# Performance work log

Measured on AMD Instinct MI355X. Metric: run time of the kernel, lower is better.

The kernel has to match this reference:

```python
import jax, jax.numpy as jnp
import numpy as np

B, N, H, C = 8, 128, 768, 5


def setup_inputs() -> dict:
    key = jax.random.key(0)
    k0, k1, k2, k3 = jax.random.split(key, 4)
    h = jax.random.normal(k0, (B, N, H), dtype=jnp.float32)
    # torch nn.Linear(4H, H): out = x @ W.T + b; we store Wcat = W.T with shape [4H, H]
    Wcat = jax.random.normal(k1, (4 * H, H), dtype=jnp.float32) * 0.02
    bW = jnp.zeros((H,), dtype=jnp.float32)
    h_hat = jax.random.normal(k2, (H,), dtype=jnp.float32)
    Wout = jax.random.normal(k3, (H, C), dtype=jnp.float32) * 0.02
    bout = jnp.zeros((C,), dtype=jnp.float32)
    return {"h": h, "Wcat": Wcat, "bW": bW, "h_hat": h_hat, "Wout": Wout, "bout": bout}


def reference(h, Wcat, bW, h_hat, Wout, bout):
    n = h.shape[1]
    W1, W2, W3, W4 = jnp.split(Wcat, 4, axis=0)  # each [H, H]
    # span order matches the torch double loop: i in range(N), j in range(i, N)
    ii, jj = jnp.triu_indices(n)  # P = n(n+1)/2
    # cat([hi,hj,hi-hj,hi*hj]) @ Wcat == hi@(W1+W3) + hj@(W2-W3) + (hi*hj)@W4
    A = jnp.einsum('bnh,hk->bnk', h, W1 + W3)   # [B, N, H]
    Bm = jnp.einsum('bnh,hk->bnk', h, W2 - W3)  # [B, N, H]
    prod = h[:, ii, :] * h[:, jj, :]            # [B, P, H]
    spans = jnp.tanh(A[:, ii, :] + Bm[:, jj, :]
                     + jnp.einsum('bph,hk->bpk', prod, W4) + bW)  # [B, P, H]
    # InterpretationLayer: attention pooling over spans
    alpha = jax.nn.softmax(jnp.einsum('bph,h->bp', spans, h_hat), axis=1)
    h_tilde = jnp.einsum('bp,bph->bh', alpha, spans)  # [B, H]
    logits = h_tilde @ Wout + bout                    # [B, C]
    return jax.nn.log_softmax(logits, axis=1)
```

## Files before the change

kernel.cpp:

```cpp
#include <hip/hip_runtime.h>
#include <hip/hip_bf16.h>


#define B_ 8
#define N_ 128
#define H_ 768
#define C_ 5
#define P_ 8256
#define TP 64
#define NBLK 129

typedef short bf16x8 __attribute__((ext_vector_type(8)));
typedef float f32x4 __attribute__((ext_vector_type(4)));

__device__ __forceinline__ float bf2f(unsigned short u){
  union { unsigned u; float f; } v; v.u = ((unsigned)u) << 16; return v.f;
}
__device__ __forceinline__ unsigned short f2bf(float f){
  union { float f; unsigned u; } v; v.f = f;
  unsigned r = v.u + 0x7FFFu + ((v.u >> 16) & 1u);
  return (unsigned short)(r >> 16);
}
__device__ __forceinline__ float tanh_fast(float x){
  float e = __expf(2.f * x);
  return 1.f - 2.f / (e + 1.f);
}
__device__ __forceinline__ int lds_off(int row, int k){
  return row * (H_ * 2) + ((k * 2) ^ ((row & 7) << 4));
}


#define PH_BLKS 3072
#define PW_BLKS 288
#define PR_BLKS 33

__global__ void prep(const float* __restrict__ h, const float* __restrict__ Wcat,
                     unsigned short* __restrict__ hb,
                     unsigned short* __restrict__ Wsum,
                     unsigned short* __restrict__ Wdif,
                     unsigned short* __restrict__ W4s,
                     int* __restrict__ ii, int* __restrict__ jj){
  const int bid = blockIdx.x;
  if (bid < PH_BLKS){
    int idx = bid * 256 + threadIdx.x;
    hb[idx] = f2bf(h[idx]);
  } else if (bid < PH_BLKS + PW_BLKS){
    int idx = (bid - PH_BLKS) * 256 + threadIdx.x;
    int o = idx / H_, col = idx % H_;
    bf16x8 vs, vd, v4;
    #pragma unroll
    for (int e = 0; e < 8; e++){
      int hrow = o * 8 + e;
      float w1 = Wcat[hrow * H_ + col];
      float w2 = Wcat[(H_ + hrow) * H_ + col];
      float w3 = Wcat[(2 * H_ + hrow) * H_ + col];
      float w4 = Wcat[(3 * H_ + hrow) * H_ + col];
      vs[e] = (short)f2bf(w1 + w3);
      vd[e] = (short)f2bf(w2 - w3);
      v4[e] = (short)f2bf(w4);
    }
    int pbase = (o * H_ + col) * 8;
    *(bf16x8*)(Wsum + pbase) = vs;
    *(bf16x8*)(Wdif + pbase) = vd;
    *(bf16x8*)(W4s + pbase)  = v4;
  } else {
    int p = (bid - PH_BLKS - PW_BLKS) * 256 + threadIdx.x;
    if (p < P_){
      int i = 0, off = 0;
      while (off + (N_ - i) <= p){ off += (N_ - i); i++; }
      ii[p] = i; jj[p] = i + (p - off);
    }
  }
}


__global__ __launch_bounds__(512, 4) void coef_gemm(
    const unsigned short* __restrict__ hb,
    const unsigned short* __restrict__ Wsum,
    const unsigned short* __restrict__ Wdif,
    const float* __restrict__ bW,
    float* __restrict__ Acoef, float* __restrict__ Bcoef){
  const int sel = blockIdx.y;
  const unsigned short* Wp = sel ? Wdif : Wsum;
  float* out = sel ? Bcoef : Acoef;
  const int growb = blockIdx.x * 16;

  __shared__ char As[16 * H_ * 2];

  const int tid = threadIdx.x;
  {
    int r = tid >> 5;
    int c = tid & 31;
    const unsigned short* src = hb + (growb + r) * H_;
    #pragma unroll
    for (int kk = 0; kk < 3; kk++){
      int k = kk * 256 + c * 8;
      bf16x8 v = *(const bf16x8*)(src + k);
      *(bf16x8*)(As + lds_off(r, k)) = v;
    }
  }
  __syncthreads();

  const int lane = tid & 63;
  const int wn = tid >> 6;
  const int hi = lane >> 4;
  const int l15 = lane & 15;
  const int colbase = wn * 96 + l15;

  f32x4 acc[6] = {};

  const bf16x8* wp = (const bf16x8*)Wp + hi * H_ + colbase;
  bf16x8 bc0 = wp[0], bc1 = wp[16], bc2 = wp[32], bc3 = wp[48], bc4 = wp[64], bc5 = wp[80];
  wp += 4 * H_;
  for (int step = 0; step < 24; ++step){
    bf16x8 bn0 = wp[0], bn1 = wp[16], bn2 = wp[32], bn3 = wp[48], bn4 = wp[64], bn5 = wp[80];
    wp += 4 * H_;
    bf16x8 a = *(const bf16x8*)(As + lds_off(l15, step * 32 + hi * 8));
    acc[0] = __builtin_amdgcn_mfma_f32_16x16x32_bf16(a, bc0, acc[0], 0, 0, 0);
    acc[1] = __builtin_amdgcn_mfma_f32_16x16x32_bf16(a, bc1, acc[1], 0, 0, 0);
    acc[2] = __builtin_amdgcn_mfma_f32_16x16x32_bf16(a, bc2, acc[2], 0, 0, 0);
    acc[3] = __builtin_amdgcn_mfma_f32_16x16x32_bf16(a, bc3, acc[3], 0, 0, 0);
    acc[4] = __builtin_amdgcn_mfma_f32_16x16x32_bf16(a, bc4, acc[4], 0, 0, 0);
    acc[5] = __builtin_amdgcn_mfma_f32_16x16x32_bf16(a, bc5, acc[5], 0, 0, 0);
    bc0 = bn0; bc1 = bn1; bc2 = bn2; bc3 = bn3; bc4 = bn4; bc5 = bn5;
  }

  #pragma unroll
  for (int ni = 0; ni < 6; ni++){
    int col = colbase + ni * 16;
    float bw = (sel == 0) ? bW[col] : 0.f;
    #pragma unroll
    for (int r = 0; r < 4; r++){
      int grow = growb + hi * 4 + r;
      out[grow * H_ + col] = acc[ni][r] + bw;
    }
  }
}


__global__ __launch_bounds__(1024)
__attribute__((amdgpu_waves_per_eu(4, 4)))
void spans_fused(
    const unsigned short* __restrict__ hb,
    const float* __restrict__ Acoef,
    const float* __restrict__ Bcoef,
    const unsigned short* __restrict__ W4s,
    const float* __restrict__ hhat,
    const int* __restrict__ ii,
    const int* __restrict__ jj,
    float* __restrict__ pm, float* __restrict__ pl, float* __restrict__ pacc){
  __shared__ char As[TP * H_ * 2];
  __shared__ int iis[TP], jjs[TP];
  __shared__ float sbuf[16][TP];
  __shared__ float wbuf[TP];

  const int bid = blockIdx.x;
  const int b = bid / NBLK;
  const int p0 = (bid % NBLK) * TP;
  const int tid = threadIdx.x;

  if (tid < TP){ iis[tid] = ii[p0 + tid]; jjs[tid] = jj[p0 + tid]; }
  __syncthreads();

  {
    int r = tid >> 4;
    int c = tid & 15;
    const unsigned short* hp = hb + (b * N_ + iis[r]) * H_;
    const unsigned short* hq = hb + (b * N_ + jjs[r]) * H_;
    #pragma unroll
    for (int kk = 0; kk < 6; kk++){
      int k = kk * 128 + c * 8;
      bf16x8 va = *(const bf16x8*)(hp + k);
      bf16x8 vb = *(const bf16x8*)(hq + k);
      bf16x8 vp;
      #pragma unroll
      for (int e = 0; e < 8; e++)
        vp[e] = (short)f2bf(bf2f((unsigned short)va[e]) * bf2f((unsigned short)vb[e]));
      *(bf16x8*)(As + lds_off(r, k)) = vp;
    }
  }

  const int lane = tid & 63;
  const int wave = tid >> 6;
  const int hi = lane >> 4;
  const int l15 = lane & 15;
  const int colbase = wave * 48 + l15;

  f32x4 acc[4][3];
  #pragma unroll
  for (int mi = 0; mi < 4; mi++){
    #pragma unroll
    for (int r = 0; r < 4; r++){
      int rowl = mi * 16 + hi * 4 + r;
      const float* ap = Acoef + (b * N_ + iis[rowl]) * H_ + colbase;
      const float* bp = Bcoef + (b * N_ + jjs[rowl]) * H_ + colbase;
      #pragma unroll
      for (int ni = 0; ni < 3; ni++)
        acc[mi][ni][r] = ap[ni * 16] + bp[ni * 16];
    }
  }
  __syncthreads();

  const bf16x8* wp = (const bf16x8*)W4s + hi * H_ + colbase;
  bf16x8 bc0 = wp[0], bc1 = wp[16], bc2 = wp[32];
  wp += 4 * H_;
  for (int step = 0; step < 24; ++step){
    bf16x8 bn0 = wp[0], bn1 = wp[16], bn2 = wp[32];
    wp += 4 * H_;
    const int kb = step * 32 + hi * 8;
    bf16x8 a0 = *(const bf16x8*)(As + lds_off(     l15, kb));
    bf16x8 a1 = *(const bf16x8*)(As + lds_off(16 + l15, kb));
    bf16x8 a2 = *(const bf16x8*)(As + lds_off(32 + l15, kb));
    bf16x8 a3 = *(const bf16x8*)(As + lds_off(48 + l15, kb));
    acc[0][0] = __builtin_amdgcn_mfma_f32_16x16x32_bf16(a0, bc0, acc[0][0], 0, 0, 0);
    acc[1][0] = __builtin_amdgcn_mfma_f32_16x16x32_bf16(a1, bc0, acc[1][0], 0, 0, 0);
    acc[2][0] = __builtin_amdgcn_mfma_f32_16x16x32_bf16(a2, bc0, acc[2][0], 0, 0, 0);
    acc[3][0] = __builtin_amdgcn_mfma_f32_16x16x32_bf16(a3, bc0, acc[3][0], 0, 0, 0);
    acc[0][1] = __builtin_amdgcn_mfma_f32_16x16x32_bf16(a0, bc1, acc[0][1], 0, 0, 0);
    acc[1][1] = __builtin_amdgcn_mfma_f32_16x16x32_bf16(a1, bc1, acc[1][1], 0, 0, 0);
    acc[2][1] = __builtin_amdgcn_mfma_f32_16x16x32_bf16(a2, bc1, acc[2][1], 0, 0, 0);
    acc[3][1] = __builtin_amdgcn_mfma_f32_16x16x32_bf16(a3, bc1, acc[3][1], 0, 0, 0);
    acc[0][2] = __builtin_amdgcn_mfma_f32_16x16x32_bf16(a0, bc2, acc[0][2], 0, 0, 0);
    acc[1][2] = __builtin_amdgcn_mfma_f32_16x16x32_bf16(a1, bc2, acc[1][2], 0, 0, 0);
    acc[2][2] = __builtin_amdgcn_mfma_f32_16x16x32_bf16(a2, bc2, acc[2][2], 0, 0, 0);
    acc[3][2] = __builtin_amdgcn_mfma_f32_16x16x32_bf16(a3, bc2, acc[3][2], 0, 0, 0);
    bc0 = bn0; bc1 = bn1; bc2 = bn2;
  }

  float sc[4][4];
  #pragma unroll
  for (int mi = 0; mi < 4; mi++)
    #pragma unroll
    for (int r = 0; r < 4; r++) sc[mi][r] = 0.f;

  #pragma unroll
  for (int ni = 0; ni < 3; ni++){
    float hh = hhat[colbase + ni * 16];
    #pragma unroll
    for (int mi = 0; mi < 4; mi++){
      #pragma unroll
      for (int r = 0; r < 4; r++){
        float s = tanh_fast(acc[mi][ni][r]);
        acc[mi][ni][r] = s;
        sc[mi][r] += s * hh;
      }
    }
  }
  #pragma unroll
  for (int mi = 0; mi < 4; mi++)
    #pragma unroll
    for (int r = 0; r < 4; r++){
      float v = sc[mi][r];
      v += __shfl_xor(v, 1); v += __shfl_xor(v, 2);
      v += __shfl_xor(v, 4); v += __shfl_xor(v, 8);
      sc[mi][r] = v;
    }
  if (l15 == 0){
    #pragma unroll
    for (int mi = 0; mi < 4; mi++)
      #pragma unroll
      for (int r = 0; r < 4; r++)
        sbuf[wave][mi * 16 + hi * 4 + r] = sc[mi][r];
  }
  __syncthreads();

  if (tid < TP){
    float s = 0.f;
    #pragma unroll
    for (int w = 0; w < 16; w++) s += sbuf[w][tid];
    float m = s;
    #pragma unroll
    for (int off = 1; off < 64; off <<= 1) m = fmaxf(m, __shfl_xor(m, off));
    float w = __expf(s - m);
    float l = w;
    #pragma unroll
    for (int off = 1; off < 64; off <<= 1) l += __shfl_xor(l, off);
    wbuf[tid] = w;
    if (tid == 0){ pm[bid] = m; pl[bid] = l; }
  }
  __syncthreads();

  #pragma unroll
  for (int ni = 0; ni < 3; ni++){
    float wa = 0.f;
    #pragma unroll
    for (int mi = 0; mi < 4; mi++)
      #pragma unroll
      for (int r = 0; r < 4; r++){
        int rowl = mi * 16 + hi * 4 + r;
        wa += wbuf[rowl] * acc[mi][ni][r];
      }
    wa += __shfl_xor(wa, 16);
    wa += __shfl_xor(wa, 32);
    if (lane < 16) pacc[bid * H_ + colbase + ni * 16] = wa;
  }
}


__global__ void merge1(
    const float* __restrict__ pm, const float* __restrict__ pl,
    const float* __restrict__ pacc, float* __restrict__ htg){
  __shared__ float ebuf[NBLK];
  __shared__ float Msh, invLsh;
  __shared__ float part[128];
  const int b = blockIdx.x;
  const int ch = blockIdx.y;
  const int tid = threadIdx.x;

  if (tid < 64){
    float m = -3.4e38f;
    for (int t = tid; t < NBLK; t += 64) m = fmaxf(m, pm[b * NBLK + t]);
    #pragma unroll
    for (int off = 1; off < 64; off <<= 1) m = fmaxf(m, __shfl_xor(m, off));
    float l = 0.f;
    for (int t = tid; t < NBLK; t += 64) l += pl[b * NBLK + t] * __expf(pm[b * NBLK + t] - m);
    #pragma unroll
    for (int off = 1; off < 64; off <<= 1) l += __shfl_xor(l, off);
    if (tid == 0){ Msh = m; invLsh = 1.f / l; }
  }
  __syncthreads();
  if (tid < NBLK) ebuf[tid] = __expf(pm[b * NBLK + tid] - Msh);
  __syncthreads();
  const int col = ch * 128 + (tid & 127);
  const int half = tid >> 7;
  float a = 0.f;
  for (int t = half; t < NBLK; t += 2) a += pacc[(b * NBLK + t) * H_ + col] * ebuf[t];
  if (half) part[tid & 127] = a;
  __syncthreads();
  if (!half) htg[b * H_ + col] = (a + part[tid]) * invLsh;
}


__global__ void merge2(
    const float* __restrict__ htg,
    const float* __restrict__ Wout, const float* __restrict__ bout,
    float* __restrict__ outp){
  const int b = blockIdx.x;
  const int lane = threadIdx.x;
  float a[C_] = {};
  for (int k = lane; k < H_; k += 64){
    float hv = htg[b * H_ + k];
    #pragma unroll
    for (int c = 0; c < C_; c++) a[c] += hv * Wout[k * C_ + c];
  }
  #pragma unroll
  for (int c = 0; c < C_; c++){
    #pragma unroll
    for (int off = 1; off < 64; off <<= 1) a[c] += __shfl_xor(a[c], off);
  }
  if (lane == 0){
    float lg[C_];
    #pragma unroll
    for (int c = 0; c < C_; c++) lg[c] = a[c] + bout[c];
    float mx = lg[0];
    #pragma unroll
    for (int c = 1; c < C_; c++) mx = fmaxf(mx, lg[c]);
    float s = 0.f;
    #pragma unroll
    for (int c = 0; c < C_; c++) s += __expf(lg[c] - mx);
    float ls = __logf(s) + mx;
    #pragma unroll
    for (int c = 0; c < C_; c++) outp[b * C_ + c] = lg[c] - ls;
  }
}


extern "C" void kernel_launch(void* const* d_in, const int* in_sizes, int n_in,
                              void* d_out, int out_size, void* d_ws, size_t ws_size,
                              hipStream_t stream){
  const float* h    = (const float*)d_in[0];
  const float* Wcat = (const float*)d_in[1];
  const float* bW   = (const float*)d_in[2];
  const float* hhat = (const float*)d_in[3];
  const float* Wout = (const float*)d_in[4];
  const float* bout = (const float*)d_in[5];
  float* outp = (float*)d_out;

  unsigned short* hb   = (unsigned short*)d_ws;
  unsigned short* Wsum = hb + 786432;
  unsigned short* Wdif = Wsum + 589824;
  unsigned short* W4s  = Wdif + 589824;
  float* Acoef = (float*)(W4s + 589824);
  float* Bcoef = Acoef + 786432;
  int* iiA = (int*)(Bcoef + 786432);
  int* jjA = iiA + P_;
  float* pm = (float*)(jjA + P_);
  float* pl = pm + (B_ * NBLK);
  float* pacc = pl + (B_ * NBLK);
  float* htg  = pacc + (B_ * NBLK * H_);

  prep<<<PH_BLKS + PW_BLKS + PR_BLKS, 256, 0, stream>>>(h, Wcat, hb, Wsum, Wdif, W4s, iiA, jjA);
  coef_gemm<<<dim3(64, 2), 512, 0, stream>>>(hb, Wsum, Wdif, bW, Acoef, Bcoef);
  spans_fused<<<B_ * NBLK, 1024, 0, stream>>>(hb, Acoef, Bcoef, W4s, hhat, iiA, jjA, pm, pl, pacc);
  merge1<<<dim3(B_, 6), 256, 0, stream>>>(pm, pl, pacc, htg);
  merge2<<<B_, 64, 0, stream>>>(htg, Wout, bout, outp);
}
```

Measured before the change: 183.6 us.

## Double-buffer span product slabs in LDS to overlap gather with MFMA

The kernel no longer builds the full 64x768 bf16 product tile in LDS before the matmul. It now splits K into three 256-wide slabs held in two LDS buffers, and loads the next slab's h rows from global memory while MFMAs run on the current one. This cuts LDS from 96KB to 64KB and hides the gather latency, at the cost of extra barriers per slab and more registers held live. The LDS swizzle also widens from 8 to 16 rows, and the launch bounds attribute is rewritten as launch_bounds(1024,4).

```diff
diff --git a/kernel.cpp b/kernel.cpp
--- a/kernel.cpp
+++ b/kernel.cpp
@@ -9,6 +9,8 @@
 #define P_ 8256
 #define TP 64
 #define NBLK 129
+#define KSLAB 256
+#define NSLAB 3
 
 typedef short bf16x8 __attribute__((ext_vector_type(8)));
 typedef float f32x4 __attribute__((ext_vector_type(4)));
@@ -26,7 +28,11 @@
   return 1.f - 2.f / (e + 1.f);
 }
 __device__ __forceinline__ int lds_off(int row, int k){
-  return row * (H_ * 2) + ((k * 2) ^ ((row & 7) << 4));
+  return row * (H_ * 2) + ((k * 2) ^ ((row & 15) << 4));
+}
+__device__ __forceinline__ int slab_off(int buf, int row, int klocal){
+  return buf * (TP * KSLAB * 2) + row * (KSLAB * 2)
+       + ((klocal * 2) ^ ((row & 15) << 4));
 }
 
 
@@ -138,8 +144,7 @@
 }
 
 
-__global__ __launch_bounds__(1024)
-__attribute__((amdgpu_waves_per_eu(4, 4)))
+__global__ __launch_bounds__(1024, 4)
 void spans_fused(
     const unsigned short* __restrict__ hb,
     const float* __restrict__ Acoef,
@@ -149,7 +154,7 @@
     const int* __restrict__ ii,
     const int* __restrict__ jj,
     float* __restrict__ pm, float* __restrict__ pl, float* __restrict__ pacc){
-  __shared__ char As[TP * H_ * 2];
+  __shared__ char As[2 * TP * KSLAB * 2];
   __shared__ int iis[TP], jjs[TP];
   __shared__ float sbuf[16][TP];
   __shared__ float wbuf[TP];
@@ -161,30 +166,22 @@
 
   if (tid < TP){ iis[tid] = ii[p0 + tid]; jjs[tid] = jj[p0 + tid]; }
   __syncthreads();
-
-  {
-    int r = tid >> 4;
-    int c = tid & 15;
-    const unsigned short* hp = hb + (b * N_ + iis[r]) * H_;
-    const unsigned short* hq = hb + (b * N_ + jjs[r]) * H_;
-    #pragma unroll
-    for (int kk = 0; kk < 6; kk++){
-      int k = kk * 128 + c * 8;
-      bf16x8 va = *(const bf16x8*)(hp + k);
-      bf16x8 vb = *(const bf16x8*)(hq + k);
-      bf16x8 vp;
-      #pragma unroll
-      for (int e = 0; e < 8; e++)
-        vp[e] = (short)f2bf(bf2f((unsigned short)va[e]) * bf2f((unsigned short)vb[e]));
-      *(bf16x8*)(As + lds_off(r, k)) = vp;
-    }
-  }
 
   const int lane = tid & 63;
   const int wave = tid >> 6;
   const int hi = lane >> 4;
   const int l15 = lane & 15;
   const int colbase = wave * 48 + l15;
+
+  const int r_st = tid >> 4;
+  const int c_st = tid & 15;
+  const unsigned short* hp = hb + (b * N_ + iis[r_st]) * H_;
+  const unsigned short* hq = hb + (b * N_ + jjs[r_st]) * H_;
+
+  bf16x8 va0 = *(const bf16x8*)(hp + c_st * 8);
+  bf16x8 va1 = *(const bf16x8*)(hp + 128 + c_st * 8);
+  bf16x8 vb0 = *(const bf16x8*)(hq + c_st * 8);
+  bf16x8 vb1 = *(const bf16x8*)(hq + 128 + c_st * 8);
 
   f32x4 acc[4][3];
   #pragma unroll
@@ -199,32 +196,68 @@
         acc[mi][ni][r] = ap[ni * 16] + bp[ni * 16];
     }
   }
+
+  {
+    bf16x8 vp0, vp1;
+    #pragma unroll
+    for (int e = 0; e < 8; e++){
+      vp0[e] = (short)f2bf(bf2f((unsigned short)va0[e]) * bf2f((unsigned short)vb0[e]));
+      vp1[e] = (short)f2bf(bf2f((unsigned short)va1[e]) * bf2f((unsigned short)vb1[e]));
+    }
+    *(bf16x8*)(As + slab_off(0, r_st, c_st * 8)) = vp0;
+    *(bf16x8*)(As + slab_off(0, r_st, 128 + c_st * 8)) = vp1;
+  }
   __syncthreads();
 
   const bf16x8* wp = (const bf16x8*)W4s + hi * H_ + colbase;
   bf16x8 bc0 = wp[0], bc1 = wp[16], bc2 = wp[32];
   wp += 4 * H_;
-  for (int step = 0; step < 24; ++step){
-    bf16x8 bn0 = wp[0], bn1 = wp[16], bn2 = wp[32];
-    wp += 4 * H_;
-    const int kb = step * 32 + hi * 8;
-    bf16x8 a0 = *(const bf16x8*)(As + lds_off(     l15, kb));
-    bf16x8 a1 = *(const bf16x8*)(As + lds_off(16 + l15, kb));
-    bf16x8 a2 = *(const bf16x8*)(As + lds_off(32 + l15, kb));
-    bf16x8 a3 = *(const bf16x8*)(As + lds_off(48 + l15, kb));
-    acc[0][0] = __builtin_amdgcn_mfma_f32_16x16x32_bf16(a0, bc0, acc[0][0], 0, 0, 0);
-    acc[1][0] = __builtin_amdgcn_mfma_f32_16x16x32_bf16(a1, bc0, acc[1][0], 0, 0, 0);
-    acc[2][0] = __builtin_amdgcn_mfma_f32_16x16x32_bf16(a2, bc0, acc[2][0], 0, 0, 0);
-    acc[3][0] = __builtin_amdgcn_mfma_f32_16x16x32_bf16(a3, bc0, acc[3][0], 0, 0, 0);
-    acc[0][1] = __builtin_amdgcn_mfma_f32_16x16x32_bf16(a0, bc1, acc[0][1], 0, 0, 0);
-    acc[1][1] = __builtin_amdgcn_mfma_f32_16x16x32_bf16(a1, bc1, acc[1][1], 0, 0, 0);
-    acc[2][1] = __builtin_amdgcn_mfma_f32_16x16x32_bf16(a2, bc1, acc[2][1], 0, 0, 0);
-    acc[3][1] = __builtin_amdgcn_mfma_f32_16x16x32_bf16(a3, bc1, acc[3][1], 0, 0, 0);
-    acc[0][2] = __builtin_amdgcn_mfma_f32_16x16x32_bf16(a0, bc2, acc[0][2], 0, 0, 0);
-    acc[1][2] = __builtin_amdgcn_mfma_f32_16x16x32_bf16(a1, bc2, acc[1][2], 0, 0, 0);
-    acc[2][2] = __builtin_amdgcn_mfma_f32_16x16x32_bf16(a2, bc2, acc[2][2], 0, 0, 0);
-    acc[3][2] = __builtin_amdgcn_mfma_f32_16x16x32_bf16(a3, bc2, acc[3][2], 0, 0, 0);
-    bc0 = bn0; bc1 = bn1; bc2 = bn2;
+
+  #pragma unroll
+  for (int slab = 0; slab < NSLAB; ++slab){
+    const int buf = slab & 1;
+    if (slab + 1 < NSLAB){
+      const int kg = (slab + 1) * KSLAB;
+      va0 = *(const bf16x8*)(hp + kg + c_st * 8);
+      va1 = *(const bf16x8*)(hp + kg + 128 + c_st * 8);
+      vb0 = *(const bf16x8*)(hq + kg + c_st * 8);
+      vb1 = *(const bf16x8*)(hq + kg + 128 + c_st * 8);
+    }
+    #pragma unroll
+    for (int st = 0; st < 8; ++st){
+      bf16x8 bn0{}, bn1{}, bn2{};
+      const bool haveNext = !(slab == NSLAB - 1 && st == 7);
+      if (haveNext){ bn0 = wp[0]; bn1 = wp[16]; bn2 = wp[32]; wp += 4 * H_; }
+      const int kl = st * 32 + hi * 8;
+      bf16x8 a0 = *(const bf16x8*)(As + slab_off(buf,      l15, kl));
+      bf16x8 a1 = *(const bf16x8*)(As + slab_off(buf, 16 + l15, kl));
+      bf16x8 a2 = *(const bf16x8*)(As + slab_off(buf, 32 + l15, kl));
+      bf16x8 a3 = *(const bf16x8*)(As + slab_off(buf, 48 + l15, kl));
+      acc[0][0] = __builtin_amdgcn_mfma_f32_16x16x32_bf16(a0, bc0, acc[0][0], 0, 0, 0);
+      acc[1][0] = __builtin_amdgcn_mfma_f32_16x16x32_bf16(a1, bc0, acc[1][0], 0, 0, 0);
+      acc[2][0] = __builtin_amdgcn_mfma_f32_16x16x32_bf16(a2, bc0, acc[2][0], 0, 0, 0);
+      acc[3][0] = __builtin_amdgcn_mfma_f32_16x16x32_bf16(a3, bc0, acc[3][0], 0, 0, 0);
+      acc[0][1] = __builtin_amdgcn_mfma_f32_16x16x32_bf16(a0, bc1, acc[0][1], 0, 0, 0);
+      acc[1][1] = __builtin_amdgcn_mfma_f32_16x16x32_bf16(a1, bc1, acc[1][1], 0, 0, 0);
+      acc[2][1] = __builtin_amdgcn_mfma_f32_16x16x32_bf16(a2, bc1, acc[2][1], 0, 0, 0);
+      acc[3][1] = __builtin_amdgcn_mfma_f32_16x16x32_bf16(a3, bc1, acc[3][1], 0, 0, 0);
+      acc[0][2] = __builtin_amdgcn_mfma_f32_16x16x32_bf16(a0, bc2, acc[0][2], 0, 0, 0);
+      acc[1][2] = __builtin_amdgcn_mfma_f32_16x16x32_bf16(a1, bc2, acc[1][2], 0, 0, 0);
+      acc[2][2] = __builtin_amdgcn_mfma_f32_16x16x32_bf16(a2, bc2, acc[2][2], 0, 0, 0);
+      acc[3][2] = __builtin_amdgcn_mfma_f32_16x16x32_bf16(a3, bc2, acc[3][2], 0, 0, 0);
+      bc0 = bn0; bc1 = bn1; bc2 = bn2;
+    }
+    if (slab + 1 < NSLAB){
+      bf16x8 vp0, vp1;
+      #pragma unroll
+      for (int e = 0; e < 8; e++){
+        vp0[e] = (short)f2bf(bf2f((unsigned short)va0[e]) * bf2f((unsigned short)vb0[e]));
+        vp1[e] = (short)f2bf(bf2f((unsigned short)va1[e]) * bf2f((unsigned short)vb1[e]));
+      }
+      *(bf16x8*)(As + slab_off(buf ^ 1, r_st, c_st * 8)) = vp0;
+      *(bf16x8*)(As + slab_off(buf ^ 1, r_st, 128 + c_st * 8)) = vp1;
+    }
+    __syncthreads();
   }
 
   float sc[4][4];
```

New measurement: 189.6 us. 1.03x slower.

## Stream W4 slabs into LDS via async global_load_lds with double-buffered product tiles

Applied to the files above, without the earlier changes.

Replaces the up-front construction of the full 64x768 product tile in LDS with a K-chunked, double-buffered pipeline. Each 32-wide K-slab of W4 is copied directly into LDS with global_load_lds while the current slab is consumed by MFMAs. The hi*hj products are now built per 128-wide chunk into a ping-pong LDS buffer, with the next chunk's loads issued ahead. The intent is to overlap weight and activation loads with matrix math, and to have each W4 slab fetched once per block into shared memory instead of per wave from global. In exchange there is a __syncthreads per step, and LDS use rises to roughly 96KB for the W4 slabs plus the product buffers. The swizzle also changes to use 16 rows, and the occupancy hint moves from waves_per_eu to launch_bounds.

```diff
diff --git a/kernel.cpp b/kernel.cpp
--- a/kernel.cpp
+++ b/kernel.cpp
@@ -9,6 +9,8 @@
 #define P_ 8256
 #define TP 64
 #define NBLK 129
+#define NSTEP 24
+#define BSLAB 49152
 
 typedef short bf16x8 __attribute__((ext_vector_type(8)));
 typedef float f32x4 __attribute__((ext_vector_type(4)));
@@ -25,8 +27,14 @@
   float e = __expf(2.f * x);
   return 1.f - 2.f / (e + 1.f);
 }
+__device__ __forceinline__ void gload_lds16(const char* g, char* l){
+  __builtin_amdgcn_global_load_lds(
+      (const __attribute__((address_space(1))) unsigned int*)g,
+      (__attribute__((address_space(3))) unsigned int*)l,
+      16, 0, 0);
+}
 __device__ __forceinline__ int lds_off(int row, int k){
-  return row * (H_ * 2) + ((k * 2) ^ ((row & 7) << 4));
+  return row * (H_ * 2) + ((k * 2) ^ ((row & 15) << 4));
 }
 
 
@@ -138,8 +146,7 @@
 }
 
 
-__global__ __launch_bounds__(1024)
-__attribute__((amdgpu_waves_per_eu(4, 4)))
+__global__ __launch_bounds__(1024, 4)
 void spans_fused(
     const unsigned short* __restrict__ hb,
     const float* __restrict__ Acoef,
@@ -149,7 +156,8 @@
     const int* __restrict__ ii,
     const int* __restrict__ jj,
     float* __restrict__ pm, float* __restrict__ pl, float* __restrict__ pacc){
-  __shared__ char As[TP * H_ * 2];
+  __shared__ char Pp[2][TP * 128 * 2];
+  __shared__ char Bsl[2][BSLAB];
   __shared__ int iis[TP], jjs[TP];
   __shared__ float sbuf[16][TP];
   __shared__ float wbuf[TP];
@@ -161,24 +169,6 @@
 
   if (tid < TP){ iis[tid] = ii[p0 + tid]; jjs[tid] = jj[p0 + tid]; }
   __syncthreads();
-
-  {
-    int r = tid >> 4;
-    int c = tid & 15;
-    const unsigned short* hp = hb + (b * N_ + iis[r]) * H_;
-    const unsigned short* hq = hb + (b * N_ + jjs[r]) * H_;
-    #pragma unroll
-    for (int kk = 0; kk < 6; kk++){
-      int k = kk * 128 + c * 8;
-      bf16x8 va = *(const bf16x8*)(hp + k);
-      bf16x8 vb = *(const bf16x8*)(hq + k);
-      bf16x8 vp;
-      #pragma unroll
-      for (int e = 0; e < 8; e++)
-        vp[e] = (short)f2bf(bf2f((unsigned short)va[e]) * bf2f((unsigned short)vb[e]));
-      *(bf16x8*)(As + lds_off(r, k)) = vp;
-    }
-  }
 
   const int lane = tid & 63;
   const int wave = tid >> 6;
@@ -186,6 +176,16 @@
   const int l15 = lane & 15;
   const int colbase = wave * 48 + l15;
 
+  const int r_st = tid >> 4;
+  const int c_st = tid & 15;
+  const unsigned short* hp = hb + (b * N_ + iis[r_st]) * H_;
+  const unsigned short* hq = hb + (b * N_ + jjs[r_st]) * H_;
+  const int pwoff = r_st * 256 + ((c_st * 16) ^ ((r_st & 15) << 4));
+  const char* wbase = (const char*)W4s;
+  const int bchunk = wave * 3072;
+
+  bf16x8 va = *(const bf16x8*)(hp + c_st * 8);
+  bf16x8 vb = *(const bf16x8*)(hq + c_st * 8);
   f32x4 acc[4][3];
   #pragma unroll
   for (int mi = 0; mi < 4; mi++){
@@ -199,32 +199,59 @@
         acc[mi][ni][r] = ap[ni * 16] + bp[ni * 16];
     }
   }
-  __syncthreads();
-
-  const bf16x8* wp = (const bf16x8*)W4s + hi * H_ + colbase;
-  bf16x8 bc0 = wp[0], bc1 = wp[16], bc2 = wp[32];
-  wp += 4 * H_;
-  for (int step = 0; step < 24; ++step){
-    bf16x8 bn0 = wp[0], bn1 = wp[16], bn2 = wp[32];
-    wp += 4 * H_;
-    const int kb = step * 32 + hi * 8;
-    bf16x8 a0 = *(const bf16x8*)(As + lds_off(     l15, kb));
-    bf16x8 a1 = *(const bf16x8*)(As + lds_off(16 + l15, kb));
-    bf16x8 a2 = *(const bf16x8*)(As + lds_off(32 + l15, kb));
-    bf16x8 a3 = *(const bf16x8*)(As + lds_off(48 + l15, kb));
-    acc[0][0] = __builtin_amdgcn_mfma_f32_16x16x32_bf16(a0, bc0, acc[0][0], 0, 0, 0);
-    acc[1][0] = __builtin_amdgcn_mfma_f32_16x16x32_bf16(a1, bc0, acc[1][0], 0, 0, 0);
-    acc[2][0] = __builtin_amdgcn_mfma_f32_16x16x32_bf16(a2, bc0, acc[2][0], 0, 0, 0);
-    acc[3][0] = __builtin_amdgcn_mfma_f32_16x16x32_bf16(a3, bc0, acc[3][0], 0, 0, 0);
-    acc[0][1] = __builtin_amdgcn_mfma_f32_16x16x32_bf16(a0, bc1, acc[0][1], 0, 0, 0);
-    acc[1][1] = __builtin_amdgcn_mfma_f32_16x16x32_bf16(a1, bc1, acc[1][1], 0, 0, 0);
-    acc[2][1] = __builtin_amdgcn_mfma_f32_16x16x32_bf16(a2, bc1, acc[2][1], 0, 0, 0);
-    acc[3][1] = __builtin_amdgcn_mfma_f32_16x16x32_bf16(a3, bc1, acc[3][1], 0, 0, 0);
-    acc[0][2] = __builtin_amdgcn_mfma_f32_16x16x32_bf16(a0, bc2, acc[0][2], 0, 0, 0);
-    acc[1][2] = __builtin_amdgcn_mfma_f32_16x16x32_bf16(a1, bc2, acc[1][2], 0, 0, 0);
-    acc[2][2] = __builtin_amdgcn_mfma_f32_16x16x32_bf16(a2, bc2, acc[2][2], 0, 0, 0);
-    acc[3][2] = __builtin_amdgcn_mfma_f32_16x16x32_bf16(a3, bc2, acc[3][2], 0, 0, 0);
-    bc0 = bn0; bc1 = bn1; bc2 = bn2;
+  {
+    bf16x8 vp;
+    #pragma unroll
+    for (int e = 0; e < 8; e++)
+      vp[e] = (short)f2bf(bf2f((unsigned short)va[e]) * bf2f((unsigned short)vb[e]));
+    *(bf16x8*)(Pp[0] + pwoff) = vp;
+  }
+  #pragma unroll
+  for (int t = 0; t < 3; t++)
+    gload_lds16(wbase + bchunk + t * 1024 + lane * 16,
+                Bsl[0] + bchunk + t * 1024);
+
+  for (int s = 0; s < NSTEP; ++s){
+    const int buf = s & 1;
+    const int pbuf = (s >> 2) & 1;
+    __syncthreads();
+
+    if (s < NSTEP - 1){
+      const char* src = wbase + (s + 1) * BSLAB + bchunk;
+      #pragma unroll
+      for (int t = 0; t < 3; t++)
+        gload_lds16(src + t * 1024 + lane * 16,
+                    Bsl[buf ^ 1] + bchunk + t * 1024);
+    }
+    if ((s & 3) == 0 && s + 4 < NSTEP){
+      const int kg = ((s >> 2) + 1) * 128;
+      va = *(const bf16x8*)(hp + kg + c_st * 8);
+      vb = *(const bf16x8*)(hq + kg + c_st * 8);
+    }
+
+    const int klb = (s & 3) * 64 + hi * 16;
+    const char* pp = Pp[pbuf];
+    bf16x8 a0 = *(const bf16x8*)(pp + (     l15) * 256 + (klb ^ (l15 << 4)));
+    bf16x8 a1 = *(const bf16x8*)(pp + (16 + l15) * 256 + (klb ^ (l15 << 4)));
+    bf16x8 a2 = *(const bf16x8*)(pp + (32 + l15) * 256 + (klb ^ (l15 << 4)));
+    bf16x8 a3 = *(const bf16x8*)(pp + (48 + l15) * 256 + (klb ^ (l15 << 4)));
+    const char* bb = Bsl[buf] + (hi * H_ + colbase) * 16;
+    #pragma unroll
+    for (int ni = 0; ni < 3; ni++){
+      bf16x8 bf = *(const bf16x8*)(bb + ni * 256);
+      acc[0][ni] = __builtin_amdgcn_mfma_f32_16x16x32_bf16(a0, bf, acc[0][ni], 0, 0, 0);
+      acc[1][ni] = __builtin_amdgcn_mfma_f32_16x16x32_bf16(a1, bf, acc[1][ni], 0, 0, 0);
+      acc[2][ni] = __builtin_amdgcn_mfma_f32_16x16x32_bf16(a2, bf, acc[2][ni], 0, 0, 0);
+      acc[3][ni] = __builtin_amdgcn_mfma_f32_16x16x32_bf16(a3, bf, acc[3][ni], 0, 0, 0);
+    }
+
+    if ((s & 3) == 3 && s < NSTEP - 1){
+      bf16x8 vp;
+      #pragma unroll
+      for (int e = 0; e < 8; e++)
+        vp[e] = (short)f2bf(bf2f((unsigned short)va[e]) * bf2f((unsigned short)vb[e]));
+      *(bf16x8*)(Pp[pbuf ^ 1] + pwoff) = vp;
+    }
   }
 
   float sc[4][4];
```

Result: slower. 199.9 us (+8.9%).

## Retile span kernel to 96-row tiles with double-buffered K-slab product staging

Applied to the files above, without the earlier changes.

The span GEMM kernel now processes 96 spans per block with 512 threads. Each wave computes a 96x96 output tile using a 6x6 accumulator grid, so W4 fragments are reused across more rows. The hi*hj product is no longer staged fully up front: it goes into LDS in 128-wide K slabs with double buffering, so the next slab is loaded and converted while the MFMAs run on the current one. A packed bf16 convert instruction, MFMA priority hints and a two-pass softmax over 96 rows are also added. The change trades higher register pressure (144 accumulator floats per lane) and fewer blocks (688 instead of 1032) for fewer W4 reloads per span.

```diff
diff --git a/kernel.cpp b/kernel.cpp
--- a/kernel.cpp
+++ b/kernel.cpp
@@ -7,8 +7,11 @@
 #define H_ 768
 #define C_ 5
 #define P_ 8256
-#define TP 64
-#define NBLK 129
+#define TP 96
+#define NBLK 86
+#define NSTEP 24
+#define SLABK 128
+#define NSLAB 6
 
 typedef short bf16x8 __attribute__((ext_vector_type(8)));
 typedef float f32x4 __attribute__((ext_vector_type(4)));
@@ -25,8 +28,20 @@
   float e = __expf(2.f * x);
   return 1.f - 2.f / (e + 1.f);
 }
+__device__ __forceinline__ bf16x8 prodpack(bf16x8 x, bf16x8 y){
+  union { bf16x8 v; unsigned u[4]; } o;
+  #pragma unroll
+  for (int e2 = 0; e2 < 4; e2++){
+    float p0 = bf2f((unsigned short)x[e2*2])   * bf2f((unsigned short)y[e2*2]);
+    float p1 = bf2f((unsigned short)x[e2*2+1]) * bf2f((unsigned short)y[e2*2+1]);
+    unsigned pk;
+    asm volatile("v_cvt_pk_bf16_f32 %0, %1, %2" : "=v"(pk) : "v"(p0), "v"(p1));
+    o.u[e2] = pk;
+  }
+  return o.v;
+}
 __device__ __forceinline__ int lds_off(int row, int k){
-  return row * (H_ * 2) + ((k * 2) ^ ((row & 7) << 4));
+  return row * (H_ * 2) + ((k * 2) ^ ((row & 15) << 4));
 }
 
 
@@ -138,8 +153,29 @@
 }
 
 
-__global__ __launch_bounds__(1024)
-__attribute__((amdgpu_waves_per_eu(4, 4)))
+#define STEP_BODY(T, BCUR, BNXT)                                             \
+  {                                                                          \
+    if ((T) + 1 < NSTEP){                                                    \
+      _Pragma("unroll")                                                      \
+      for (int ni = 0; ni < 6; ni++)                                         \
+        BNXT[ni] = wp[(((T) + 1) * 4 + hi) * H_ + colbase + ni * 16];        \
+    }                                                                        \
+    const int klb = ((T) & 3) * 64 + hi * 16;                                \
+    bf16x8 a[6];                                                             \
+    _Pragma("unroll")                                                        \
+    for (int mg = 0; mg < 6; mg++)                                           \
+      a[mg] = *(const bf16x8*)(pcur + (mg * 16 + l15) * 256 + (klb ^ (l15 << 4))); \
+    __builtin_amdgcn_s_setprio(1);                                           \
+    _Pragma("unroll")                                                        \
+    for (int ni = 0; ni < 6; ni++){                                          \
+      _Pragma("unroll")                                                      \
+      for (int mg = 0; mg < 6; mg++)                                         \
+        acc[mg][ni] = __builtin_amdgcn_mfma_f32_16x16x32_bf16(a[mg], BCUR[ni], acc[mg][ni], 0, 0, 0); \
+    }                                                                        \
+    __builtin_amdgcn_s_setprio(0);                                           \
+  }
+
+__global__ __launch_bounds__(512, 2)
 void spans_fused(
     const unsigned short* __restrict__ hb,
     const float* __restrict__ Acoef,
@@ -149,10 +185,11 @@
     const int* __restrict__ ii,
     const int* __restrict__ jj,
     float* __restrict__ pm, float* __restrict__ pl, float* __restrict__ pacc){
-  __shared__ char As[TP * H_ * 2];
+  __shared__ char Pp[2][TP * 256];
   __shared__ int iis[TP], jjs[TP];
-  __shared__ float sbuf[16][TP];
+  __shared__ float sbuf[8][TP];
   __shared__ float wbuf[TP];
+  __shared__ float Msh;
 
   const int bid = blockIdx.x;
   const int b = bid / NBLK;
@@ -162,134 +199,147 @@
   if (tid < TP){ iis[tid] = ii[p0 + tid]; jjs[tid] = jj[p0 + tid]; }
   __syncthreads();
 
-  {
-    int r = tid >> 4;
-    int c = tid & 15;
-    const unsigned short* hp = hb + (b * N_ + iis[r]) * H_;
-    const unsigned short* hq = hb + (b * N_ + jjs[r]) * H_;
-    #pragma unroll
-    for (int kk = 0; kk < 6; kk++){
-      int k = kk * 128 + c * 8;
-      bf16x8 va = *(const bf16x8*)(hp + k);
-      bf16x8 vb = *(const bf16x8*)(hq + k);
-      bf16x8 vp;
-      #pragma unroll
-      for (int e = 0; e < 8; e++)
-        vp[e] = (short)f2bf(bf2f((unsigned short)va[e]) * bf2f((unsigned short)vb[e]));
-      *(bf16x8*)(As + lds_off(r, k)) = vp;
-    }
-  }
-
   const int lane = tid & 63;
   const int wave = tid >> 6;
   const int hi = lane >> 4;
   const int l15 = lane & 15;
-  const int colbase = wave * 48 + l15;
-
-  f32x4 acc[4][3];
-  #pragma unroll
-  for (int mi = 0; mi < 4; mi++){
+  const int colbase = wave * 96 + l15;
+
+  int rch[3], cch[3];
+  const unsigned short *hpr[3], *hqr[3];
+  #pragma unroll
+  for (int t = 0; t < 3; t++){
+    int cid = tid + t * 512;
+    rch[t] = cid >> 4; cch[t] = cid & 15;
+    hpr[t] = hb + (b * N_ + iis[rch[t]]) * H_;
+    hqr[t] = hb + (b * N_ + jjs[rch[t]]) * H_;
+  }
+
+  bf16x8 va[3], vb[3];
+  #pragma unroll
+  for (int t = 0; t < 3; t++){
+    va[t] = *(const bf16x8*)(hpr[t] + cch[t] * 8);
+    vb[t] = *(const bf16x8*)(hqr[t] + cch[t] * 8);
+  }
+
+  f32x4 acc[6][6];
+  #pragma unroll
+  for (int mg = 0; mg < 6; mg++){
     #pragma unroll
     for (int r = 0; r < 4; r++){
-      int rowl = mi * 16 + hi * 4 + r;
+      int rowl = mg * 16 + hi * 4 + r;
       const float* ap = Acoef + (b * N_ + iis[rowl]) * H_ + colbase;
       const float* bp = Bcoef + (b * N_ + jjs[rowl]) * H_ + colbase;
       #pragma unroll
-      for (int ni = 0; ni < 3; ni++)
-        acc[mi][ni][r] = ap[ni * 16] + bp[ni * 16];
-    }
-  }
-  __syncthreads();
-
-  const bf16x8* wp = (const bf16x8*)W4s + hi * H_ + colbase;
-  bf16x8 bc0 = wp[0], bc1 = wp[16], bc2 = wp[32];
-  wp += 4 * H_;
-  for (int step = 0; step < 24; ++step){
-    bf16x8 bn0 = wp[0], bn1 = wp[16], bn2 = wp[32];
-    wp += 4 * H_;
-    const int kb = step * 32 + hi * 8;
-    bf16x8 a0 = *(const bf16x8*)(As + lds_off(     l15, kb));
-    bf16x8 a1 = *(const bf16x8*)(As + lds_off(16 + l15, kb));
-    bf16x8 a2 = *(const bf16x8*)(As + lds_off(32 + l15, kb));
-    bf16x8 a3 = *(const bf16x8*)(As + lds_off(48 + l15, kb));
-    acc[0][0] = __builtin_amdgcn_mfma_f32_16x16x32_bf16(a0, bc0, acc[0][0], 0, 0, 0);
-    acc[1][0] = __builtin_amdgcn_mfma_f32_16x16x32_bf16(a1, bc0, acc[1][0], 0, 0, 0);
-    acc[2][0] = __builtin_amdgcn_mfma_f32_16x16x32_bf16(a2, bc0, acc[2][0], 0, 0, 0);
-    acc[3][0] = __builtin_amdgcn_mfma_f32_16x16x32_bf16(a3, bc0, acc[3][0], 0, 0, 0);
-    acc[0][1] = __builtin_amdgcn_mfma_f32_16x16x32_bf16(a0, bc1, acc[0][1], 0, 0, 0);
-    acc[1][1] = __builtin_amdgcn_mfma_f32_16x16x32_bf16(a1, bc1, acc[1][1], 0, 0, 0);
-    acc[2][1] = __builtin_amdgcn_mfma_f32_16x16x32_bf16(a2, bc1, acc[2][1], 0, 0, 0);
-    acc[3][1] = __builtin_amdgcn_mfma_f32_16x16x32_bf16(a3, bc1, acc[3][1], 0, 0, 0);
-    acc[0][2] = __builtin_amdgcn_mfma_f32_16x16x32_bf16(a0, bc2, acc[0][2], 0, 0, 0);
-    acc[1][2] = __builtin_amdgcn_mfma_f32_16x16x32_bf16(a1, bc2, acc[1][2], 0, 0, 0);
-    acc[2][2] = __builtin_amdgcn_mfma_f32_16x16x32_bf16(a2, bc2, acc[2][2], 0, 0, 0);
-    acc[3][2] = __builtin_amdgcn_mfma_f32_16x16x32_bf16(a3, bc2, acc[3][2], 0, 0, 0);
-    bc0 = bn0; bc1 = bn1; bc2 = bn2;
-  }
-
-  float sc[4][4];
-  #pragma unroll
-  for (int mi = 0; mi < 4; mi++)
-    #pragma unroll
-    for (int r = 0; r < 4; r++) sc[mi][r] = 0.f;
-
-  #pragma unroll
-  for (int ni = 0; ni < 3; ni++){
+      for (int ni = 0; ni < 6; ni++)
+        acc[mg][ni][r] = ap[ni * 16] + bp[ni * 16];
+    }
+  }
+
+  #pragma unroll
+  for (int t = 0; t < 3; t++)
+    *(bf16x8*)(Pp[0] + rch[t] * 256 + ((cch[t] * 16) ^ ((rch[t] & 15) << 4))) =
+        prodpack(va[t], vb[t]);
+
+  const bf16x8* wp = (const bf16x8*)W4s;
+  bf16x8 bA[6], bB[6];
+  #pragma unroll
+  for (int ni = 0; ni < 6; ni++)
+    bA[ni] = wp[hi * H_ + colbase + ni * 16];
+
+  __syncthreads();
+
+  for (int slab = 0; slab < NSLAB; ++slab){
+    const char* pcur = Pp[slab & 1];
+    if (slab + 1 < NSLAB){
+      const int kg = (slab + 1) * SLABK;
+      #pragma unroll
+      for (int t = 0; t < 3; t++){
+        va[t] = *(const bf16x8*)(hpr[t] + kg + cch[t] * 8);
+        vb[t] = *(const bf16x8*)(hqr[t] + kg + cch[t] * 8);
+      }
+    }
+    const int t0 = slab * 4;
+    STEP_BODY(t0,     bA, bB);
+    STEP_BODY(t0 + 1, bB, bA);
+    STEP_BODY(t0 + 2, bA, bB);
+    STEP_BODY(t0 + 3, bB, bA);
+    if (slab + 1 < NSLAB){
+      #pragma unroll
+      for (int t = 0; t < 3; t++)
+        *(bf16x8*)(Pp[(slab & 1) ^ 1] + rch[t] * 256 +
+                   ((cch[t] * 16) ^ ((rch[t] & 15) << 4))) = prodpack(va[t], vb[t]);
+    }
+    __syncthreads();
+  }
+
+  float sc[6][4];
+  #pragma unroll
+  for (int mg = 0; mg < 6; mg++)
+    #pragma unroll
+    for (int r = 0; r < 4; r++) sc[mg][r] = 0.f;
+
+  #pragma unroll
+  for (int ni = 0; ni < 6; ni++){
     float hh = hhat[colbase + ni * 16];
     #pragma unroll
-    for (int mi = 0; mi < 4; mi++){
+    for (int mg = 0; mg < 6; mg++){
       #pragma unroll
       for (int r = 0; r < 4; r++){
-        float s = tanh_fast(acc[mi][ni][r]);
-        acc[mi][ni][r] = s;
-        sc[mi][r] += s * hh;
+        float s = tanh_fast(acc[mg][ni][r]);
+        acc[mg][ni][r] = s;
+        sc[mg][r] += s * hh;
       }
     }
   }
   #pragma unroll
-  for (int mi = 0; mi < 4; mi++)
+  for (int mg = 0; mg < 6; mg++)
     #pragma unroll
     for (int r = 0; r < 4; r++){
-      float v = sc[mi][r];
+      float v = sc[mg][r];
       v += __shfl_xor(v, 1); v += __shfl_xor(v, 2);
       v += __shfl_xor(v, 4); v += __shfl_xor(v, 8);
-      sc[mi][r] = v;
+      sc[mg][r] = v;
     }
   if (l15 == 0){
     #pragma unroll
-    for (int mi = 0; mi < 4; mi++)
+    for (int mg = 0; mg < 6; mg++)
       #pragma unroll
       for (int r = 0; r < 4; r++)
-        sbuf[wave][mi * 16 + hi * 4 + r] = sc[mi][r];
+        sbuf[wave][mg * 16 + hi * 4 + r] = sc[mg][r];
   }
   __syncthreads();
 
   if (tid < TP){
     float s = 0.f;
     #pragma unroll
-    for (int w = 0; w < 16; w++) s += sbuf[w][tid];
-    float m = s;
+    for (int w = 0; w < 8; w++) s += sbuf[w][tid];
+    wbuf[tid] = s;
+  }
+  __syncthreads();
+  if (tid < 64){
+    float a = wbuf[tid];
+    float bq = (tid < 32) ? wbuf[64 + tid] : -3.4e38f;
+    float m = fmaxf(a, bq);
     #pragma unroll
     for (int off = 1; off < 64; off <<= 1) m = fmaxf(m, __shfl_xor(m, off));
-    float w = __expf(s - m);
-    float l = w;
+    float l = __expf(a - m) + ((tid < 32) ? __expf(bq - m) : 0.f);
     #pragma unroll
     for (int off = 1; off < 64; off <<= 1) l += __shfl_xor(l, off);
-    wbuf[tid] = w;
-    if (tid == 0){ pm[bid] = m; pl[bid] = l; }
-  }
-  __syncthreads();
-
-  #pragma unroll
-  for (int ni = 0; ni < 3; ni++){
+    if (tid == 0){ pm[bid] = m; pl[bid] = l; Msh = m; }
+  }
+  __syncthreads();
+  if (tid < TP) wbuf[tid] = __expf(wbuf[tid] - Msh);
+  __syncthreads();
+
+  #pragma unroll
+  for (int ni = 0; ni < 6; ni++){
     float wa = 0.f;
     #pragma unroll
-    for (int mi = 0; mi < 4; mi++)
-      #pragma unroll
-      for (int r = 0; r < 4; r++){
-        int rowl = mi * 16 + hi * 4 + r;
-        wa += wbuf[rowl] * acc[mi][ni][r];
-      }
+    for (int mg = 0; mg < 6; mg++)
+      #pragma unroll
+      for (int r = 0; r < 4; r++)
+        wa += wbuf[mg * 16 + hi * 4 + r] * acc[mg][ni][r];
     wa += __shfl_xor(wa, 16);
     wa += __shfl_xor(wa, 32);
     if (lane < 16) pacc[bid * H_ + colbase + ni * 16] = wa;
@@ -391,7 +441,7 @@
 
   prep<<<PH_BLKS + PW_BLKS + PR_BLKS, 256, 0, stream>>>(h, Wcat, hb, Wsum, Wdif, W4s, iiA, jjA);
   coef_gemm<<<dim3(64, 2), 512, 0, stream>>>(hb, Wsum, Wdif, bW, Acoef, Bcoef);
-  spans_fused<<<B_ * NBLK, 1024, 0, stream>>>(hb, Acoef, Bcoef, W4s, hhat, iiA, jjA, pm, pl, pacc);
+  spans_fused<<<B_ * NBLK, 512, 0, stream>>>(hb, Acoef, Bcoef, W4s, hhat, iiA, jjA, pm, pl, pacc);
   merge1<<<dim3(B_, 6), 256, 0, stream>>>(pm, pl, pacc, htg);
   merge2<<<B_, 64, 0, stream>>>(htg, Wout, bout, outp);
 }
```

After: 188.9 us. 1.03x slower.
